# Optimization experiments

Hardware: AMD Instinct MI355X
Metric: run time of the kernel (lower is better)

Reference implementation:

```python
import jax, jax.numpy as jnp
import numpy as np

N_NODES = 10000
N_EDGES = 640000
IN_CH, HID, OUT_CH = 128, 128, 64


def _gcn_conv(x, edge_index, edge_weight, W, b, n_nodes):
    # PyG GCNConv (default add_self_loops=True, normalize=True, bias=True):
    #   A_hat = A + I ; D = rowsum(A_hat) ; norm_e = D^-1/2[src] * w_e * D^-1/2[dst]
    #   out[dst] += norm_e * (x @ W)[src] ; out += b
    src, dst = edge_index[0], edge_index[1]
    loop = jnp.arange(n_nodes, dtype=edge_index.dtype)
    src = jnp.concatenate([src, loop])
    dst = jnp.concatenate([dst, loop])
    w = jnp.concatenate([edge_weight, jnp.ones((n_nodes,), edge_weight.dtype)])
    deg = jax.ops.segment_sum(w, dst, num_segments=n_nodes)  # scatter on col
    dinv = jnp.where(deg > 0, jax.lax.rsqrt(deg), 0.0).astype(x.dtype)
    norm = dinv[src] * w * dinv[dst]  # [E+N]
    xw = x @ W  # dense GEMM [N, out]
    msg = norm[:, None] * xw[src]  # gather + scale [E+N, out]
    out = jax.ops.segment_sum(msg, dst, num_segments=n_nodes)  # scatter-add
    return out + b


def setup_inputs() -> dict:
    key = jax.random.key(0)
    ks = jax.random.split(key, 8)
    x = jax.random.normal(ks[0], (N_NODES, IN_CH), dtype=jnp.float32)
    edge_index = jax.random.randint(ks[1], (2, N_EDGES), 0, N_NODES, dtype=jnp.int64)
    edge_weight = jax.random.uniform(ks[2], (N_EDGES,), dtype=jnp.float32)
    W1 = jax.random.normal(ks[3], (IN_CH, HID), dtype=jnp.float32) * 0.05
    b1 = jnp.zeros((HID,), jnp.float32)
    W2 = jax.random.normal(ks[4], (HID, OUT_CH), dtype=jnp.float32) * 0.05
    b2 = jnp.zeros((OUT_CH,), jnp.float32)
    return {"x": x, "edge_index": edge_index, "edge_weight": edge_weight,
            "W1": W1, "b1": b1, "W2": W2, "b2": b2}


def reference(x, edge_index, edge_weight, W1, b1, W2, b2):
    h = _gcn_conv(x, edge_index, edge_weight, W1, b1, N_NODES)
    h = jax.nn.relu(h)
    out = _gcn_conv(h, edge_index, edge_weight, W2, b2, N_NODES)
    return out
```

## Files before the change

### kernel.cpp

```cpp
#include <hip/hip_runtime.h>
#include <math.h>

#define N_NODES 10000
#define N_EDGES 640000
#define ELLW    192

#define CHUNKS  128
#define CHUNK_E 5000
#define GB      625

typedef unsigned long long ull;
typedef unsigned int uint;
typedef unsigned short ushort;
typedef unsigned char uchar;

#define FIXED_SCALE 262144.0f


__device__ __forceinline__ float bf_lo(uint u) { return __uint_as_float(u << 16); }
__device__ __forceinline__ float bf_hi(uint u) { return __uint_as_float(u & 0xffff0000u); }
__device__ __forceinline__ ushort f2bf(float v) {
    uint u = __float_as_uint(v);
    uint r = u + 0x7fffu + ((u >> 16) & 1u);
    return (ushort)(r >> 16);
}

__global__ __launch_bounds__(256) void kernelA(const int* __restrict__ ei,
                                               const float* __restrict__ ew,
                                               uint* __restrict__ sd32,
                                               uint* __restrict__ blockcnt,
                                               const float* __restrict__ x,
                                               const float* __restrict__ W1,
                                               ushort* __restrict__ xw1b) {
    __shared__ uint smem[N_NODES];
    const int tid = threadIdx.x;
    if (blockIdx.x < CHUNKS) {
        const int c = blockIdx.x;
        __shared__ int sflag;
        if (tid == 0) sflag = 0;
        for (int i = tid; i < N_NODES; i += 256) smem[i] = 0u;
        __syncthreads();
        int a = (tid < 64) ? ei[2 * (c * CHUNK_E + tid) + 1] : 0;
        if (a) atomicOr(&sflag, 1);
        __syncthreads();
        const int f = sflag;
        const ull* ei64 = (const ull*)ei;
        for (int k = tid; k < CHUNK_E; k += 256) {
            int e = c * CHUNK_E + k;
            int s, d;
            if (f) { s = ei[e];        d = ei[N_EDGES + e]; }
            else   { s = (int)ei64[e]; d = (int)ei64[N_EDGES + e]; }
            float w = ew[e];
            uint fx = (uint)(w * FIXED_SCALE + 0.5f);
            uint old = atomicAdd(&smem[d], (1u << 24) | fx);
            uint r = (old >> 24) & 15u;
            sd32[e] = (r << 28) | ((uint)d << 14) | (uint)s;
        }
        __syncthreads();
        for (int i = tid; i < N_NODES; i += 256)
            blockcnt[c * N_NODES + i] = smem[i];
    } else {
        constexpr int K = 128, TM = 16, KT = 32, NCOL = 128, RPT = 8;
        float* sA = (float*)smem;
        float* sB = sA + TM * (KT + 1);
        int blk = blockIdx.x - CHUNKS;
        int c = tid % NCOL, rr = tid / NCOL;
        int row0 = blk * TM;
        float acc[RPT];
#pragma unroll
        for (int r = 0; r < RPT; ++r) acc[r] = 0.0f;
        for (int k0 = 0; k0 < K; k0 += KT) {
            for (int i = tid; i < TM * KT; i += 256) {
                int r = i / KT, k = i % KT;
                int gr = row0 + r;
                sA[r * (KT + 1) + k] = (gr < N_NODES) ? x[gr * K + k0 + k] : 0.0f;
            }
            for (int i = tid; i < KT * NCOL; i += 256) {
                int k = i / NCOL, cc = i % NCOL;
                sB[k * NCOL + cc] = W1[(k0 + k) * NCOL + cc];
            }
            __syncthreads();
#pragma unroll
            for (int k = 0; k < KT; ++k) {
                float b = sB[k * NCOL + c];
#pragma unroll
                for (int r = 0; r < RPT; ++r)
                    acc[r] += sA[(rr * RPT + r) * (KT + 1) + k] * b;
            }
            __syncthreads();
        }
#pragma unroll
        for (int r = 0; r < RPT; ++r) {
            int gr = row0 + rr * RPT + r;
            if (gr < N_NODES) xw1b[gr * NCOL + c] = f2bf(acc[r]);
        }
    }
}

__global__ __launch_bounds__(256) void scanB(const uint* __restrict__ blockcnt,
                                             uchar* __restrict__ base8,
                                             int* __restrict__ cnt_arr,
                                             float* __restrict__ dinv,
                                             const float* __restrict__ W2,
                                             uint* __restrict__ w2pg) {
    if (blockIdx.x >= 40) {
        int i = (blockIdx.x - 40) * 256 + threadIdx.x;
        int k2 = i >> 6, cc = i & 63;
        uint lo = (uint)f2bf(W2[(2 * k2) * 64 + cc]);
        uint hi = (uint)f2bf(W2[(2 * k2 + 1) * 64 + cc]);
        w2pg[i] = lo | (hi << 16);
        return;
    }
    int n = blockIdx.x * 256 + threadIdx.x;
    if (n >= N_NODES) return;
    uint wsum = 0;
    int run = 0;
#pragma unroll 8
    for (int c = 0; c < CHUNKS; ++c) {
        uint v = blockcnt[c * N_NODES + n];
        base8[c * N_NODES + n] = (uchar)run;
        run += (int)(v >> 24);
        wsum += v & 0xffffffu;
    }
    cnt_arr[n] = run;
    float dg = 1.0f + (float)wsum * (1.0f / FIXED_SCALE);
    dinv[n] = (float)(1.0 / sqrt((double)dg));
}

__global__ __launch_bounds__(256) void fillC(const uint* __restrict__ sd32,
                                             const float* __restrict__ ew,
                                             const uchar* __restrict__ base8,
                                             const float* __restrict__ dinv,
                                             ull* __restrict__ epack) {
    const int gid = blockIdx.x * 256 + threadIdx.x;
    const int stride = gridDim.x * 256;
    for (int e = gid; e < N_EDGES; e += stride) {
        uint sd = sd32[e];
        int s = (int)(sd & 0x3fffu);
        int d = (int)((sd >> 14) & 0x3fffu);
        int r = (int)(sd >> 28);
        int c = e / CHUNK_E;
        float nrm = dinv[s] * ew[e] * dinv[d];
        int slot = (int)base8[c * N_NODES + d] + r;
        if (slot < ELLW)
            epack[d * ELLW + slot] = ((ull)__float_as_uint(nrm) << 32) | (ull)(uint)s;
    }
}

__global__ __launch_bounds__(256, 8) void aggC(const ushort* __restrict__ xw1b,
                                               const ull* __restrict__ epack,
                                               const int* __restrict__ cnt_arr,
                                               const float* __restrict__ dinv,
                                               const float* __restrict__ b1,
                                               const uint* __restrict__ w2pg,
                                               ushort* __restrict__ xw2b) {
    __shared__ float hl[4][128];
    __shared__ uint w2p[64 * 64];
    const uint* __restrict__ xw32 = (const uint*)xw1b;
    const int tid = threadIdx.x;
    int l = tid & 63;
    int wv = tid >> 6;
    int node = blockIdx.x * 4 + wv;

    for (int i = tid; i < 64 * 64; i += 256) w2p[i] = w2pg[i];

    int cnt = __builtin_amdgcn_readfirstlane(cnt_arr[node]);
    if (cnt > ELLW) cnt = ELLW;
    float dn = dinv[node];
    float d2 = dn * dn;
    uint su = xw32[node * 64 + l];
    float acc0 = d2 * bf_lo(su);
    float acc1 = d2 * bf_hi(su);
    const ull* ep = epack + (long)node * ELLW;
    int j = 0;
    for (; j + 8 <= cnt; j += 8) {
        ulonglong2 v0 = *(const ulonglong2*)(ep + j);
        ulonglong2 v1 = *(const ulonglong2*)(ep + j + 2);
        ulonglong2 v2 = *(const ulonglong2*)(ep + j + 4);
        ulonglong2 v3 = *(const ulonglong2*)(ep + j + 6);
        uint u0 = xw32[(uint)v0.x * 64 + l];
        uint u1 = xw32[(uint)v0.y * 64 + l];
        uint u2 = xw32[(uint)v1.x * 64 + l];
        uint u3 = xw32[(uint)v1.y * 64 + l];
        uint u4 = xw32[(uint)v2.x * 64 + l];
        uint u5 = xw32[(uint)v2.y * 64 + l];
        uint u6 = xw32[(uint)v3.x * 64 + l];
        uint u7 = xw32[(uint)v3.y * 64 + l];
        float n0 = __uint_as_float((uint)(v0.x >> 32));
        float n1 = __uint_as_float((uint)(v0.y >> 32));
        float n2 = __uint_as_float((uint)(v1.x >> 32));
        float n3 = __uint_as_float((uint)(v1.y >> 32));
        float n4 = __uint_as_float((uint)(v2.x >> 32));
        float n5 = __uint_as_float((uint)(v2.y >> 32));
        float n6 = __uint_as_float((uint)(v3.x >> 32));
        float n7 = __uint_as_float((uint)(v3.y >> 32));
        acc0 = fmaf(n0, bf_lo(u0), acc0); acc1 = fmaf(n0, bf_hi(u0), acc1);
        acc0 = fmaf(n1, bf_lo(u1), acc0); acc1 = fmaf(n1, bf_hi(u1), acc1);
        acc0 = fmaf(n2, bf_lo(u2), acc0); acc1 = fmaf(n2, bf_hi(u2), acc1);
        acc0 = fmaf(n3, bf_lo(u3), acc0); acc1 = fmaf(n3, bf_hi(u3), acc1);
        acc0 = fmaf(n4, bf_lo(u4), acc0); acc1 = fmaf(n4, bf_hi(u4), acc1);
        acc0 = fmaf(n5, bf_lo(u5), acc0); acc1 = fmaf(n5, bf_hi(u5), acc1);
        acc0 = fmaf(n6, bf_lo(u6), acc0); acc1 = fmaf(n6, bf_hi(u6), acc1);
        acc0 = fmaf(n7, bf_lo(u7), acc0); acc1 = fmaf(n7, bf_hi(u7), acc1);
    }
    for (; j + 2 <= cnt; j += 2) {
        ulonglong2 vv = *(const ulonglong2*)(ep + j);
        uint u0 = xw32[(uint)vv.x * 64 + l];
        uint u1 = xw32[(uint)vv.y * 64 + l];
        float n0 = __uint_as_float((uint)(vv.x >> 32));
        float n1 = __uint_as_float((uint)(vv.y >> 32));
        acc0 = fmaf(n0, bf_lo(u0), acc0); acc1 = fmaf(n0, bf_hi(u0), acc1);
        acc0 = fmaf(n1, bf_lo(u1), acc0); acc1 = fmaf(n1, bf_hi(u1), acc1);
    }
    if (j < cnt) {
        ull v = ep[j];
        uint u = xw32[(uint)v * 64 + l];
        float n = __uint_as_float((uint)(v >> 32));
        acc0 = fmaf(n, bf_lo(u), acc0);
        acc1 = fmaf(n, bf_hi(u), acc1);
    }
    float2 bb = ((const float2*)b1)[l];
    hl[wv][2 * l]     = fmaxf(acc0 + bb.x, 0.0f);
    hl[wv][2 * l + 1] = fmaxf(acc1 + bb.y, 0.0f);
    __syncthreads();

    float acc = 0.0f;
#pragma unroll 8
    for (int k2 = 0; k2 < 64; ++k2) {
        uint w = w2p[k2 * 64 + l];
        acc = fmaf(hl[wv][2 * k2],     bf_lo(w), acc);
        acc = fmaf(hl[wv][2 * k2 + 1], bf_hi(w), acc);
    }
    xw2b[node * 64 + l] = f2bf(acc);
}

__global__ __launch_bounds__(256) void agg2(const ushort* __restrict__ xw2b,
                                            const ull* __restrict__ epack,
                                            const int* __restrict__ cnt_arr,
                                            const float* __restrict__ dinv,
                                            const float* __restrict__ b2,
                                            float* __restrict__ out) {
    const uint* __restrict__ xw32 = (const uint*)xw2b;
    int lane = threadIdx.x & 63;
    int half = lane >> 5;
    int q = lane & 31;
    int pair = blockIdx.x * 4 + (threadIdx.x >> 6);
    int A = pair * 2, B = A + 1;
    int cntA = __builtin_amdgcn_readfirstlane(cnt_arr[A]);
    int cntB = __builtin_amdgcn_readfirstlane(cnt_arr[B]);
    if (cntA > ELLW) cntA = ELLW;
    if (cntB > ELLW) cntB = ELLW;
    int myn = half ? B : A;
    int mycnt = half ? cntB : cntA;
    float dn = dinv[myn];
    float d2 = dn * dn;
    uint su = xw32[myn * 32 + q];
    float acc0 = d2 * bf_lo(su);
    float acc1 = d2 * bf_hi(su);
    const ull* epA = epack + (long)A * ELLW;
    const ull* epB = epack + (long)B * ELLW;
    int mx = cntA > cntB ? cntA : cntB;
    int j = 0;
    for (; j + 8 <= mx; j += 8) {
        ulonglong2 a0 = *(const ulonglong2*)(epA + j);
        ulonglong2 a1 = *(const ulonglong2*)(epA + j + 2);
        ulonglong2 a2 = *(const ulonglong2*)(epA + j + 4);
        ulonglong2 a3 = *(const ulonglong2*)(epA + j + 6);
        ulonglong2 b0 = *(const ulonglong2*)(epB + j);
        ulonglong2 b1v = *(const ulonglong2*)(epB + j + 2);
        ulonglong2 b2v = *(const ulonglong2*)(epB + j + 4);
        ulonglong2 b3 = *(const ulonglong2*)(epB + j + 6);
        ull e0 = half ? b0.x : a0.x;
        ull e1 = half ? b0.y : a0.y;
        ull e2 = half ? b1v.x : a1.x;
        ull e3 = half ? b1v.y : a1.y;
        ull e4 = half ? b2v.x : a2.x;
        ull e5 = half ? b2v.y : a2.y;
        ull e6 = half ? b3.x : a3.x;
        ull e7 = half ? b3.y : a3.y;
        uint u0 = xw32[((uint)e0 & 0xffffu) * 32 + q];
        uint u1 = xw32[((uint)e1 & 0xffffu) * 32 + q];
        uint u2 = xw32[((uint)e2 & 0xffffu) * 32 + q];
        uint u3 = xw32[((uint)e3 & 0xffffu) * 32 + q];
        uint u4 = xw32[((uint)e4 & 0xffffu) * 32 + q];
        uint u5 = xw32[((uint)e5 & 0xffffu) * 32 + q];
        uint u6 = xw32[((uint)e6 & 0xffffu) * 32 + q];
        uint u7 = xw32[((uint)e7 & 0xffffu) * 32 + q];
        float n0 = (j     < mycnt) ? __uint_as_float((uint)(e0 >> 32)) : 0.0f;
        float n1 = (j + 1 < mycnt) ? __uint_as_float((uint)(e1 >> 32)) : 0.0f;
        float n2 = (j + 2 < mycnt) ? __uint_as_float((uint)(e2 >> 32)) : 0.0f;
        float n3 = (j + 3 < mycnt) ? __uint_as_float((uint)(e3 >> 32)) : 0.0f;
        float n4 = (j + 4 < mycnt) ? __uint_as_float((uint)(e4 >> 32)) : 0.0f;
        float n5 = (j + 5 < mycnt) ? __uint_as_float((uint)(e5 >> 32)) : 0.0f;
        float n6 = (j + 6 < mycnt) ? __uint_as_float((uint)(e6 >> 32)) : 0.0f;
        float n7 = (j + 7 < mycnt) ? __uint_as_float((uint)(e7 >> 32)) : 0.0f;
        acc0 = fmaf(n0, bf_lo(u0), acc0); acc1 = fmaf(n0, bf_hi(u0), acc1);
        acc0 = fmaf(n1, bf_lo(u1), acc0); acc1 = fmaf(n1, bf_hi(u1), acc1);
        acc0 = fmaf(n2, bf_lo(u2), acc0); acc1 = fmaf(n2, bf_hi(u2), acc1);
        acc0 = fmaf(n3, bf_lo(u3), acc0); acc1 = fmaf(n3, bf_hi(u3), acc1);
        acc0 = fmaf(n4, bf_lo(u4), acc0); acc1 = fmaf(n4, bf_hi(u4), acc1);
        acc0 = fmaf(n5, bf_lo(u5), acc0); acc1 = fmaf(n5, bf_hi(u5), acc1);
        acc0 = fmaf(n6, bf_lo(u6), acc0); acc1 = fmaf(n6, bf_hi(u6), acc1);
        acc0 = fmaf(n7, bf_lo(u7), acc0); acc1 = fmaf(n7, bf_hi(u7), acc1);
    }
    for (; j < mx; ++j) {
        ull vA = epA[j], vB = epB[j];
        ull v = half ? vB : vA;
        uint s = (uint)v & 0xffffu;
        float n = (j < mycnt) ? __uint_as_float((uint)(v >> 32)) : 0.0f;
        uint u = xw32[s * 32 + q];
        acc0 = fmaf(n, bf_lo(u), acc0);
        acc1 = fmaf(n, bf_hi(u), acc1);
    }
    float2 bb = ((const float2*)b2)[q];
    float2 o;
    o.x = acc0 + bb.x;
    o.y = acc1 + bb.y;
    ((float2*)out)[myn * 32 + q] = o;
}

extern "C" void kernel_launch(void* const* d_in, const int* in_sizes, int n_in,
                              void* d_out, int out_size, void* d_ws, size_t ws_size,
                              hipStream_t stream) {
    const float* x  = (const float*)d_in[0];
    const int*   ei = (const int*)d_in[1];
    const float* ew = (const float*)d_in[2];
    const float* W1 = (const float*)d_in[3];
    const float* b1 = (const float*)d_in[4];
    const float* W2 = (const float*)d_in[5];
    const float* b2 = (const float*)d_in[6];
    float* out = (float*)d_out;

    char* ws = (char*)d_ws;
    ushort* xw1b    = (ushort*)(ws + 0);
    ushort* xw2b    = (ushort*)(ws + 5120000);
    ull*    epack   = (ull*)   (ws + 6400000);
    uint*   blockcnt= (uint*)  (ws + 21760000);
    uchar*  base8   = (uchar*) (ws + 26880000);
    uint*   sd32    = (uint*)  (ws + 28800000);
    int*    cnt_arr = (int*)   (ws + 31360000);
    float*  dinv    = (float*) (ws + 31400000);
    uint*   w2pg    = (uint*)  (ws + 31440000);

    kernelA<<<CHUNKS + GB, 256, 0, stream>>>(ei, ew, sd32, blockcnt, x, W1, xw1b);
    scanB<<<56, 256, 0, stream>>>(blockcnt, base8, cnt_arr, dinv, W2, w2pg);
    fillC<<<512, 256, 0, stream>>>(sd32, ew, base8, dinv, epack);
    aggC<<<2500, 256, 0, stream>>>(xw1b, epack, cnt_arr, dinv, b1, w2pg, xw2b);
    agg2<<<1250, 256, 0, stream>>>(xw2b, epack, cnt_arr, dinv, b2, out);
}
```

Baseline: 156.4 us.

## Split edges across lane groups with 16-byte gathers in both aggregation kernels

Both aggregation kernels now assign one node per wavefront. Lane groups each take different edges and gather whole 16-byte chunks of the bf16 feature row, then combine partial sums with cross-lane xor shuffles. Edge-pack reads are prefetched one iteration ahead. The aim is fewer, wider gather loads and more independent edges in flight. Alongside this, the first-layer GEMM reads its A tile as float4 from a padded LDS layout, and the fill and second-layer grids plus aggC's occupancy hint are retuned. The cost is extra shuffle reductions and padded tail iterations that load unused slots with their weight set to zero.

```diff
diff --git a/kernel.cpp b/kernel.cpp
--- a/kernel.cpp
+++ b/kernel.cpp
@@ -24,6 +24,12 @@
     uint r = u + 0x7fffu + ((u >> 16) & 1u);
     return (ushort)(r >> 16);
 }
+
+#define ACC8(n, r) \
+    acc[0] = fmaf(n, bf_lo((r).x), acc[0]); acc[1] = fmaf(n, bf_hi((r).x), acc[1]); \
+    acc[2] = fmaf(n, bf_lo((r).y), acc[2]); acc[3] = fmaf(n, bf_hi((r).y), acc[3]); \
+    acc[4] = fmaf(n, bf_lo((r).z), acc[4]); acc[5] = fmaf(n, bf_hi((r).z), acc[5]); \
+    acc[6] = fmaf(n, bf_lo((r).w), acc[6]); acc[7] = fmaf(n, bf_hi((r).w), acc[7]);
 
 __global__ __launch_bounds__(256) void kernelA(const int* __restrict__ ei,
                                                const float* __restrict__ ew,
@@ -32,7 +38,7 @@
                                                const float* __restrict__ x,
                                                const float* __restrict__ W1,
                                                ushort* __restrict__ xw1b) {
-    __shared__ uint smem[N_NODES];
+    __shared__ __align__(16) uint smem[N_NODES];
     const int tid = threadIdx.x;
     if (blockIdx.x < CHUNKS) {
         const int c = blockIdx.x;
@@ -60,9 +66,9 @@
         for (int i = tid; i < N_NODES; i += 256)
             blockcnt[c * N_NODES + i] = smem[i];
     } else {
-        constexpr int K = 128, TM = 16, KT = 32, NCOL = 128, RPT = 8;
+        constexpr int K = 128, TM = 16, KT = 32, NCOL = 128, RPT = 8, LDA = KT + 4;
         float* sA = (float*)smem;
-        float* sB = sA + TM * (KT + 1);
+        float* sB = sA + TM * LDA;
         int blk = blockIdx.x - CHUNKS;
         int c = tid % NCOL, rr = tid / NCOL;
         int row0 = blk * TM;
@@ -73,7 +79,7 @@
             for (int i = tid; i < TM * KT; i += 256) {
                 int r = i / KT, k = i % KT;
                 int gr = row0 + r;
-                sA[r * (KT + 1) + k] = (gr < N_NODES) ? x[gr * K + k0 + k] : 0.0f;
+                sA[r * LDA + k] = (gr < N_NODES) ? x[gr * K + k0 + k] : 0.0f;
             }
             for (int i = tid; i < KT * NCOL; i += 256) {
                 int k = i / NCOL, cc = i % NCOL;
@@ -81,11 +87,19 @@
             }
             __syncthreads();
 #pragma unroll
-            for (int k = 0; k < KT; ++k) {
-                float b = sB[k * NCOL + c];
-#pragma unroll
-                for (int r = 0; r < RPT; ++r)
-                    acc[r] += sA[(rr * RPT + r) * (KT + 1) + k] * b;
+            for (int k = 0; k < KT; k += 4) {
+                float b0 = sB[(k + 0) * NCOL + c];
+                float b1 = sB[(k + 1) * NCOL + c];
+                float b2 = sB[(k + 2) * NCOL + c];
+                float b3 = sB[(k + 3) * NCOL + c];
+#pragma unroll
+                for (int r = 0; r < RPT; ++r) {
+                    const float4 av = *(const float4*)&sA[(rr * RPT + r) * LDA + k];
+                    acc[r] = fmaf(av.x, b0, acc[r]);
+                    acc[r] = fmaf(av.y, b1, acc[r]);
+                    acc[r] = fmaf(av.z, b2, acc[r]);
+                    acc[r] = fmaf(av.w, b3, acc[r]);
+                }
             }
             __syncthreads();
         }
@@ -147,7 +161,7 @@
     }
 }
 
-__global__ __launch_bounds__(256, 8) void aggC(const ushort* __restrict__ xw1b,
+__global__ __launch_bounds__(256, 6) void aggC(const ushort* __restrict__ xw1b,
                                                const ull* __restrict__ epack,
                                                const int* __restrict__ cnt_arr,
                                                const float* __restrict__ dinv,
@@ -158,165 +172,142 @@
     __shared__ uint w2p[64 * 64];
     const uint* __restrict__ xw32 = (const uint*)xw1b;
     const int tid = threadIdx.x;
-    int l = tid & 63;
-    int wv = tid >> 6;
-    int node = blockIdx.x * 4 + wv;
-
-    for (int i = tid; i < 64 * 64; i += 256) w2p[i] = w2pg[i];
+    const int l = tid & 63;
+    const int wv = tid >> 6;
+    const int g = l >> 4;
+    const int q = l & 15;
+    const int node = blockIdx.x * 4 + wv;
 
     int cnt = __builtin_amdgcn_readfirstlane(cnt_arr[node]);
     if (cnt > ELLW) cnt = ELLW;
+    const ull* ep = epack + (long)node * ELLW;
+
+    ulonglong2 eA = *(const ulonglong2*)(ep + 2 * g);
+    ulonglong2 eB = *(const ulonglong2*)(ep + 8 + 2 * g);
+
+    for (int i = tid; i < 64 * 64; i += 256) w2p[i] = w2pg[i];
+
+    float acc[8];
+#pragma unroll
+    for (int i = 0; i < 8; ++i) acc[i] = 0.0f;
+
+    for (int j = 0; j < cnt; j += 16) {
+        ulonglong2 nA = *(const ulonglong2*)(ep + j + 16 + 2 * g);
+        ulonglong2 nB = *(const ulonglong2*)(ep + j + 24 + 2 * g);
+        uint s0 = (uint)eA.x & 0x3fffu;
+        uint s1 = (uint)eA.y & 0x3fffu;
+        uint s2 = (uint)eB.x & 0x3fffu;
+        uint s3 = (uint)eB.y & 0x3fffu;
+        uint4 r0 = *(const uint4*)(xw32 + s0 * 64 + q * 4);
+        uint4 r1 = *(const uint4*)(xw32 + s1 * 64 + q * 4);
+        uint4 r2 = *(const uint4*)(xw32 + s2 * 64 + q * 4);
+        uint4 r3 = *(const uint4*)(xw32 + s3 * 64 + q * 4);
+        float n0 = (j + 2 * g     < cnt) ? __uint_as_float((uint)(eA.x >> 32)) : 0.0f;
+        float n1 = (j + 2 * g + 1 < cnt) ? __uint_as_float((uint)(eA.y >> 32)) : 0.0f;
+        float n2 = (j + 2 * g + 8 < cnt) ? __uint_as_float((uint)(eB.x >> 32)) : 0.0f;
+        float n3 = (j + 2 * g + 9 < cnt) ? __uint_as_float((uint)(eB.y >> 32)) : 0.0f;
+        ACC8(n0, r0)
+        ACC8(n1, r1)
+        ACC8(n2, r2)
+        ACC8(n3, r3)
+        eA = nA; eB = nB;
+    }
+
+#pragma unroll
+    for (int i = 0; i < 8; ++i) {
+        acc[i] += __shfl_xor(acc[i], 16, 64);
+        acc[i] += __shfl_xor(acc[i], 32, 64);
+    }
+
     float dn = dinv[node];
     float d2 = dn * dn;
-    uint su = xw32[node * 64 + l];
-    float acc0 = d2 * bf_lo(su);
-    float acc1 = d2 * bf_hi(su);
-    const ull* ep = epack + (long)node * ELLW;
-    int j = 0;
-    for (; j + 8 <= cnt; j += 8) {
-        ulonglong2 v0 = *(const ulonglong2*)(ep + j);
-        ulonglong2 v1 = *(const ulonglong2*)(ep + j + 2);
-        ulonglong2 v2 = *(const ulonglong2*)(ep + j + 4);
-        ulonglong2 v3 = *(const ulonglong2*)(ep + j + 6);
-        uint u0 = xw32[(uint)v0.x * 64 + l];
-        uint u1 = xw32[(uint)v0.y * 64 + l];
-        uint u2 = xw32[(uint)v1.x * 64 + l];
-        uint u3 = xw32[(uint)v1.y * 64 + l];
-        uint u4 = xw32[(uint)v2.x * 64 + l];
-        uint u5 = xw32[(uint)v2.y * 64 + l];
-        uint u6 = xw32[(uint)v3.x * 64 + l];
-        uint u7 = xw32[(uint)v3.y * 64 + l];
-        float n0 = __uint_as_float((uint)(v0.x >> 32));
-        float n1 = __uint_as_float((uint)(v0.y >> 32));
-        float n2 = __uint_as_float((uint)(v1.x >> 32));
-        float n3 = __uint_as_float((uint)(v1.y >> 32));
-        float n4 = __uint_as_float((uint)(v2.x >> 32));
-        float n5 = __uint_as_float((uint)(v2.y >> 32));
-        float n6 = __uint_as_float((uint)(v3.x >> 32));
-        float n7 = __uint_as_float((uint)(v3.y >> 32));
-        acc0 = fmaf(n0, bf_lo(u0), acc0); acc1 = fmaf(n0, bf_hi(u0), acc1);
-        acc0 = fmaf(n1, bf_lo(u1), acc0); acc1 = fmaf(n1, bf_hi(u1), acc1);
-        acc0 = fmaf(n2, bf_lo(u2), acc0); acc1 = fmaf(n2, bf_hi(u2), acc1);
-        acc0 = fmaf(n3, bf_lo(u3), acc0); acc1 = fmaf(n3, bf_hi(u3), acc1);
-        acc0 = fmaf(n4, bf_lo(u4), acc0); acc1 = fmaf(n4, bf_hi(u4), acc1);
-        acc0 = fmaf(n5, bf_lo(u5), acc0); acc1 = fmaf(n5, bf_hi(u5), acc1);
-        acc0 = fmaf(n6, bf_lo(u6), acc0); acc1 = fmaf(n6, bf_hi(u6), acc1);
-        acc0 = fmaf(n7, bf_lo(u7), acc0); acc1 = fmaf(n7, bf_hi(u7), acc1);
-    }
-    for (; j + 2 <= cnt; j += 2) {
-        ulonglong2 vv = *(const ulonglong2*)(ep + j);
-        uint u0 = xw32[(uint)vv.x * 64 + l];
-        uint u1 = xw32[(uint)vv.y * 64 + l];
-        float n0 = __uint_as_float((uint)(vv.x >> 32));
-        float n1 = __uint_as_float((uint)(vv.y >> 32));
-        acc0 = fmaf(n0, bf_lo(u0), acc0); acc1 = fmaf(n0, bf_hi(u0), acc1);
-        acc0 = fmaf(n1, bf_lo(u1), acc0); acc1 = fmaf(n1, bf_hi(u1), acc1);
-    }
-    if (j < cnt) {
-        ull v = ep[j];
-        uint u = xw32[(uint)v * 64 + l];
-        float n = __uint_as_float((uint)(v >> 32));
-        acc0 = fmaf(n, bf_lo(u), acc0);
-        acc1 = fmaf(n, bf_hi(u), acc1);
-    }
-    float2 bb = ((const float2*)b1)[l];
-    hl[wv][2 * l]     = fmaxf(acc0 + bb.x, 0.0f);
-    hl[wv][2 * l + 1] = fmaxf(acc1 + bb.y, 0.0f);
+    uint4 sv = *(const uint4*)(xw32 + node * 64 + q * 4);
+    float4 b1a = *(const float4*)(b1 + 8 * q);
+    float4 b1b = *(const float4*)(b1 + 8 * q + 4);
+    if (g == 0) {
+        hl[wv][8 * q + 0] = fmaxf(acc[0] + d2 * bf_lo(sv.x) + b1a.x, 0.0f);
+        hl[wv][8 * q + 1] = fmaxf(acc[1] + d2 * bf_hi(sv.x) + b1a.y, 0.0f);
+        hl[wv][8 * q + 2] = fmaxf(acc[2] + d2 * bf_lo(sv.y) + b1a.z, 0.0f);
+        hl[wv][8 * q + 3] = fmaxf(acc[3] + d2 * bf_hi(sv.y) + b1a.w, 0.0f);
+        hl[wv][8 * q + 4] = fmaxf(acc[4] + d2 * bf_lo(sv.z) + b1b.x, 0.0f);
+        hl[wv][8 * q + 5] = fmaxf(acc[5] + d2 * bf_hi(sv.z) + b1b.y, 0.0f);
+        hl[wv][8 * q + 6] = fmaxf(acc[6] + d2 * bf_lo(sv.w) + b1b.z, 0.0f);
+        hl[wv][8 * q + 7] = fmaxf(acc[7] + d2 * bf_hi(sv.w) + b1b.w, 0.0f);
+    }
     __syncthreads();
 
-    float acc = 0.0f;
+    float acc2 = 0.0f;
 #pragma unroll 8
     for (int k2 = 0; k2 < 64; ++k2) {
         uint w = w2p[k2 * 64 + l];
-        acc = fmaf(hl[wv][2 * k2],     bf_lo(w), acc);
-        acc = fmaf(hl[wv][2 * k2 + 1], bf_hi(w), acc);
-    }
-    xw2b[node * 64 + l] = f2bf(acc);
-}
-
-__global__ __launch_bounds__(256) void agg2(const ushort* __restrict__ xw2b,
-                                            const ull* __restrict__ epack,
-                                            const int* __restrict__ cnt_arr,
-                                            const float* __restrict__ dinv,
-                                            const float* __restrict__ b2,
-                                            float* __restrict__ out) {
+        acc2 = fmaf(hl[wv][2 * k2],     bf_lo(w), acc2);
+        acc2 = fmaf(hl[wv][2 * k2 + 1], bf_hi(w), acc2);
+    }
+    xw2b[node * 64 + l] = f2bf(acc2);
+}
+
+__global__ __launch_bounds__(256, 8) void agg2(const ushort* __restrict__ xw2b,
+                                               const ull* __restrict__ epack,
+                                               const int* __restrict__ cnt_arr,
+                                               const float* __restrict__ dinv,
+                                               const float* __restrict__ b2,
+                                               float* __restrict__ out) {
     const uint* __restrict__ xw32 = (const uint*)xw2b;
-    int lane = threadIdx.x & 63;
-    int half = lane >> 5;
-    int q = lane & 31;
-    int pair = blockIdx.x * 4 + (threadIdx.x >> 6);
-    int A = pair * 2, B = A + 1;
-    int cntA = __builtin_amdgcn_readfirstlane(cnt_arr[A]);
-    int cntB = __builtin_amdgcn_readfirstlane(cnt_arr[B]);
-    if (cntA > ELLW) cntA = ELLW;
-    if (cntB > ELLW) cntB = ELLW;
-    int myn = half ? B : A;
-    int mycnt = half ? cntB : cntA;
-    float dn = dinv[myn];
+    const int tid = threadIdx.x;
+    const int l = tid & 63;
+    const int wv = tid >> 6;
+    const int g = l >> 3;
+    const int q = l & 7;
+    const int node = blockIdx.x * 4 + wv;
+
+    int cnt = __builtin_amdgcn_readfirstlane(cnt_arr[node]);
+    if (cnt > ELLW) cnt = ELLW;
+    const ull* ep = epack + (long)node * ELLW;
+
+    ulonglong2 eA = *(const ulonglong2*)(ep + 2 * g);
+
+    float acc[8];
+#pragma unroll
+    for (int i = 0; i < 8; ++i) acc[i] = 0.0f;
+
+    for (int j = 0; j < cnt; j += 16) {
+        ulonglong2 nA = *(const ulonglong2*)(ep + j + 16 + 2 * g);
+        uint s0 = (uint)eA.x & 0x3fffu;
+        uint s1 = (uint)eA.y & 0x3fffu;
+        uint4 r0 = *(const uint4*)(xw32 + s0 * 32 + q * 4);
+        uint4 r1 = *(const uint4*)(xw32 + s1 * 32 + q * 4);
+        float n0 = (j + 2 * g     < cnt) ? __uint_as_float((uint)(eA.x >> 32)) : 0.0f;
+        float n1 = (j + 2 * g + 1 < cnt) ? __uint_as_float((uint)(eA.y >> 32)) : 0.0f;
+        ACC8(n0, r0)
+        ACC8(n1, r1)
+        eA = nA;
+    }
+
+#pragma unroll
+    for (int i = 0; i < 8; ++i) {
+        acc[i] += __shfl_xor(acc[i], 8, 64);
+        acc[i] += __shfl_xor(acc[i], 16, 64);
+        acc[i] += __shfl_xor(acc[i], 32, 64);
+    }
+
+    float dn = dinv[node];
     float d2 = dn * dn;
-    uint su = xw32[myn * 32 + q];
-    float acc0 = d2 * bf_lo(su);
-    float acc1 = d2 * bf_hi(su);
-    const ull* epA = epack + (long)A * ELLW;
-    const ull* epB = epack + (long)B * ELLW;
-    int mx = cntA > cntB ? cntA : cntB;
-    int j = 0;
-    for (; j + 8 <= mx; j += 8) {
-        ulonglong2 a0 = *(const ulonglong2*)(epA + j);
-        ulonglong2 a1 = *(const ulonglong2*)(epA + j + 2);
-        ulonglong2 a2 = *(const ulonglong2*)(epA + j + 4);
-        ulonglong2 a3 = *(const ulonglong2*)(epA + j + 6);
-        ulonglong2 b0 = *(const ulonglong2*)(epB + j);
-        ulonglong2 b1v = *(const ulonglong2*)(epB + j + 2);
-        ulonglong2 b2v = *(const ulonglong2*)(epB + j + 4);
-        ulonglong2 b3 = *(const ulonglong2*)(epB + j + 6);
-        ull e0 = half ? b0.x : a0.x;
-        ull e1 = half ? b0.y : a0.y;
-        ull e2 = half ? b1v.x : a1.x;
-        ull e3 = half ? b1v.y : a1.y;
-        ull e4 = half ? b2v.x : a2.x;
-        ull e5 = half ? b2v.y : a2.y;
-        ull e6 = half ? b3.x : a3.x;
-        ull e7 = half ? b3.y : a3.y;
-        uint u0 = xw32[((uint)e0 & 0xffffu) * 32 + q];
-        uint u1 = xw32[((uint)e1 & 0xffffu) * 32 + q];
-        uint u2 = xw32[((uint)e2 & 0xffffu) * 32 + q];
-        uint u3 = xw32[((uint)e3 & 0xffffu) * 32 + q];
-        uint u4 = xw32[((uint)e4 & 0xffffu) * 32 + q];
-        uint u5 = xw32[((uint)e5 & 0xffffu) * 32 + q];
-        uint u6 = xw32[((uint)e6 & 0xffffu) * 32 + q];
-        uint u7 = xw32[((uint)e7 & 0xffffu) * 32 + q];
-        float n0 = (j     < mycnt) ? __uint_as_float((uint)(e0 >> 32)) : 0.0f;
-        float n1 = (j + 1 < mycnt) ? __uint_as_float((uint)(e1 >> 32)) : 0.0f;
-        float n2 = (j + 2 < mycnt) ? __uint_as_float((uint)(e2 >> 32)) : 0.0f;
-        float n3 = (j + 3 < mycnt) ? __uint_as_float((uint)(e3 >> 32)) : 0.0f;
-        float n4 = (j + 4 < mycnt) ? __uint_as_float((uint)(e4 >> 32)) : 0.0f;
-        float n5 = (j + 5 < mycnt) ? __uint_as_float((uint)(e5 >> 32)) : 0.0f;
-        float n6 = (j + 6 < mycnt) ? __uint_as_float((uint)(e6 >> 32)) : 0.0f;
-        float n7 = (j + 7 < mycnt) ? __uint_as_float((uint)(e7 >> 32)) : 0.0f;
-        acc0 = fmaf(n0, bf_lo(u0), acc0); acc1 = fmaf(n0, bf_hi(u0), acc1);
-        acc0 = fmaf(n1, bf_lo(u1), acc0); acc1 = fmaf(n1, bf_hi(u1), acc1);
-        acc0 = fmaf(n2, bf_lo(u2), acc0); acc1 = fmaf(n2, bf_hi(u2), acc1);
-        acc0 = fmaf(n3, bf_lo(u3), acc0); acc1 = fmaf(n3, bf_hi(u3), acc1);
-        acc0 = fmaf(n4, bf_lo(u4), acc0); acc1 = fmaf(n4, bf_hi(u4), acc1);
-        acc0 = fmaf(n5, bf_lo(u5), acc0); acc1 = fmaf(n5, bf_hi(u5), acc1);
-        acc0 = fmaf(n6, bf_lo(u6), acc0); acc1 = fmaf(n6, bf_hi(u6), acc1);
-        acc0 = fmaf(n7, bf_lo(u7), acc0); acc1 = fmaf(n7, bf_hi(u7), acc1);
-    }
-    for (; j < mx; ++j) {
-        ull vA = epA[j], vB = epB[j];
-        ull v = half ? vB : vA;
-        uint s = (uint)v & 0xffffu;
-        float n = (j < mycnt) ? __uint_as_float((uint)(v >> 32)) : 0.0f;
-        uint u = xw32[s * 32 + q];
-        acc0 = fmaf(n, bf_lo(u), acc0);
-        acc1 = fmaf(n, bf_hi(u), acc1);
-    }
-    float2 bb = ((const float2*)b2)[q];
-    float2 o;
-    o.x = acc0 + bb.x;
-    o.y = acc1 + bb.y;
-    ((float2*)out)[myn * 32 + q] = o;
+    uint4 sv = *(const uint4*)(xw32 + node * 32 + q * 4);
+    float4 b2a = *(const float4*)(b2 + 8 * q);
+    float4 b2b = *(const float4*)(b2 + 8 * q + 4);
+    if (g == 0) {
+        float4 oa, ob;
+        oa.x = acc[0] + d2 * bf_lo(sv.x) + b2a.x;
+        oa.y = acc[1] + d2 * bf_hi(sv.x) + b2a.y;
+        oa.z = acc[2] + d2 * bf_lo(sv.y) + b2a.z;
+        oa.w = acc[3] + d2 * bf_hi(sv.y) + b2a.w;
+        ob.x = acc[4] + d2 * bf_lo(sv.z) + b2b.x;
+        ob.y = acc[5] + d2 * bf_hi(sv.z) + b2b.y;
+        ob.z = acc[6] + d2 * bf_lo(sv.w) + b2b.z;
+        ob.w = acc[7] + d2 * bf_hi(sv.w) + b2b.w;
+        *(float4*)(out + node * 64 + 8 * q)     = oa;
+        *(float4*)(out + node * 64 + 8 * q + 4) = ob;
+    }
 }
 
 extern "C" void kernel_launch(void* const* d_in, const int* in_sizes, int n_in,
@@ -344,7 +335,7 @@
 
     kernelA<<<CHUNKS + GB, 256, 0, stream>>>(ei, ew, sd32, blockcnt, x, W1, xw1b);
     scanB<<<56, 256, 0, stream>>>(blockcnt, base8, cnt_arr, dinv, W2, w2pg);
-    fillC<<<512, 256, 0, stream>>>(sd32, ew, base8, dinv, epack);
+    fillC<<<2500, 256, 0, stream>>>(sd32, ew, base8, dinv, epack);
     aggC<<<2500, 256, 0, stream>>>(xw1b, epack, cnt_arr, dinv, b1, w2pg, xw2b);
-    agg2<<<1250, 256, 0, stream>>>(xw2b, epack, cnt_arr, dinv, b2, out);
-}
+    agg2<<<2500, 256, 0, stream>>>(xw2b, epack, cnt_arr, dinv, b2, out);
+}
```

Measured after the change: 139.4 us. 1.12x faster.
